# Kernel optimization log

Measured on AMD Instinct MI355X. Metric: run time of the kernel, lower is better.

The kernel has to match this reference:

```python
import jax, jax.numpy as jnp
import numpy as np

N_NODES = 50000
N_EDGES = 800000
N_FEAT = 128
HIDDEN = 64
N_GRAPHS = 256


def setup_inputs() -> dict:
    key = jax.random.key(0)
    ks = jax.random.split(key, 10)
    x = jax.random.normal(ks[0], (N_NODES, N_FEAT), dtype=jnp.float32)
    edge_index = jax.random.randint(ks[1], (2, N_EDGES), 0, N_NODES, dtype=jnp.int64)
    batch = jnp.sort(jax.random.randint(ks[2], (N_NODES,), 0, N_GRAPHS, dtype=jnp.int64))
    s1 = 1.0 / np.sqrt(N_FEAT)
    s2 = 1.0 / np.sqrt(HIDDEN)
    W1 = jax.random.normal(ks[3], (N_FEAT, HIDDEN), dtype=jnp.float32) * s1
    b1 = jnp.zeros((HIDDEN,), dtype=jnp.float32)
    W2 = jax.random.normal(ks[4], (HIDDEN, HIDDEN), dtype=jnp.float32) * s2
    b2 = jnp.zeros((HIDDEN,), dtype=jnp.float32)
    Wm1 = jax.random.normal(ks[5], (HIDDEN, HIDDEN), dtype=jnp.float32) * s2
    bm1 = jnp.zeros((HIDDEN,), dtype=jnp.float32)
    Wm2 = jax.random.normal(ks[6], (HIDDEN, 1), dtype=jnp.float32) * s2
    bm2 = jnp.zeros((1,), dtype=jnp.float32)
    return {"x": x, "edge_index": edge_index, "batch": batch,
            "W1": W1, "b1": b1, "W2": W2, "b2": b2,
            "Wm1": Wm1, "bm1": bm1, "Wm2": Wm2, "bm2": bm2}


def _gcn_layer(h, W, b, src, dst, norm, n_nodes):
    # GCNConv: h @ W, then symmetric-normalized scatter-add over edges (+ self-loops), + bias
    h = h @ W
    msg = h[src] * norm[:, None]              # [E+N, H] gather + scale
    agg = jax.ops.segment_sum(msg, dst, num_segments=n_nodes)
    return agg + b


def reference(x, edge_index, batch, W1, b1, W2, b2, Wm1, bm1, Wm2, bm2):
    n = x.shape[0]
    loops = jnp.arange(n, dtype=edge_index.dtype)
    src = jnp.concatenate([edge_index[0], loops])  # self-loops as in PyG GCNConv
    dst = jnp.concatenate([edge_index[1], loops])
    deg = jax.ops.segment_sum(jnp.ones_like(dst, dtype=x.dtype), dst, num_segments=n)
    dis = jnp.where(deg > 0, jax.lax.rsqrt(deg), 0.0)  # deg^-1/2
    norm = dis[src] * dis[dst]

    h = jax.nn.relu(_gcn_layer(x, W1, b1, src, dst, norm, n))
    h = jax.nn.relu(_gcn_layer(h, W2, b2, src, dst, norm, n))

    # global mean pool over graphs
    sums = jax.ops.segment_sum(h, batch, num_segments=N_GRAPHS)
    cnts = jax.ops.segment_sum(jnp.ones((n,), dtype=h.dtype), batch, num_segments=N_GRAPHS)
    pooled = sums / jnp.maximum(cnts, 1.0)[:, None]

    # MLP head (dropout inactive at eval)
    out = jax.nn.relu(pooled @ Wm1 + bm1) @ Wm2 + bm2
    return out.reshape(-1)
```

## Files before the change

kernel.cpp:

```cpp
#include <hip/hip_runtime.h>

#define NN 50000
#define NE 800000
#define NF 128
#define NH 64
#define NG 256
#define NB 196
#define NC 196
#define CH 4096
#define CELL 80
#define CAP 5120
#define NGB 782

typedef __attribute__((ext_vector_type(8))) short bf16x8;
typedef __attribute__((ext_vector_type(4))) float f32x4;

static __device__ __forceinline__ unsigned short f2bf(float f) {
    union { float f; unsigned u; } v; v.f = f;
    unsigned r = v.u + 0x7FFF + ((v.u >> 16) & 1);
    return (unsigned short)(r >> 16);
}
static __device__ __forceinline__ float lo16(unsigned u) {
    return __uint_as_float(u << 16);
}
static __device__ __forceinline__ float hi16(unsigned u) {
    return __uint_as_float(u & 0xFFFF0000u);
}
static __device__ __forceinline__ unsigned pack2(float a, float b) {
    return (unsigned)f2bf(a) | ((unsigned)f2bf(b) << 16);
}

__global__ __launch_bounds__(256) void prep_gemm(const int* __restrict__ ei,
                                                 int* __restrict__ histg,
                                                 int2* __restrict__ ebuf,
                                                 const float* __restrict__ X,
                                                 const float* __restrict__ W,
                                                 unsigned short* __restrict__ Y,
                                                 float* __restrict__ psum) {
    __shared__ __align__(16) char smem[35840];
    const int t = threadIdx.x;

    if (blockIdx.x < NC) {
        int* hist = (int*)smem;
        int* incl = hist + 256;
        int* lcur = incl + 256;
        int2* lpairs = (int2*)(smem + 3072);
        const int c = blockIdx.x;
        const int c0 = c * CH;

        hist[t] = 0;
        __syncthreads();

        int2 loc[16];
#pragma unroll
        for (int j = 0; j < 16; ++j) {
            int e = c0 + j * 256 + t;
            int s = -1, d = -1;
            if (e < NE) {
                s = ei[e]; d = ei[NE + e];
                atomicAdd(&hist[d >> 8], 1);
            }
            loc[j] = make_int2(s, d);
        }
        __syncthreads();

        int v = hist[t];
        incl[t] = v;
        __syncthreads();
        for (int off = 1; off < 256; off <<= 1) {
            int u = (t >= off) ? incl[t - off] : 0;
            __syncthreads();
            incl[t] += u;
            __syncthreads();
        }
        lcur[t] = incl[t] - v;
        if (t < NB) histg[c * NB + t] = v;
        __syncthreads();

#pragma unroll
        for (int j = 0; j < 16; ++j) {
            int d = loc[j].y;
            if (d >= 0) {
                int p = atomicAdd(&lcur[d >> 8], 1);
                lpairs[p] = loc[j];
            }
        }
        __syncthreads();

        const int total = incl[255];
        for (int p = t; p < total; p += 256) {
            int2 pr = lpairs[p];
            int b = pr.y >> 8;
            int i = p - (incl[b] - hist[b]);
            ebuf[(b * NC + c) * CELL + i] = pr;
        }
    } else {
        const int gb = blockIdx.x - NC;
        if (gb < 16)
            *(float4*)&psum[gb * 1024 + t * 4] = make_float4(0.f, 0.f, 0.f, 0.f);

        unsigned short* Xs = (unsigned short*)smem;
        unsigned int* Wt = (unsigned int*)(smem + 17408);
        const int base = gb * 64;

        for (int i = t * 4; i < 64 * 128; i += 1024) {
            int node = i >> 7, k = i & 127;
            int gn = base + node; if (gn >= NN) gn = NN - 1;
            float4 v = *(const float4*)&X[(size_t)gn * 128 + k];
            ushort4 o = { f2bf(v.x), f2bf(v.y), f2bf(v.z), f2bf(v.w) };
            *(ushort4*)&Xs[node * 136 + k] = o;
        }
        for (int idx = t; idx < 64 * 64; idx += 256) {
            int n = idx & 63, kp = idx >> 6;
            float w0 = W[(2 * kp) * 64 + n];
            float w1 = W[(2 * kp + 1) * 64 + n];
            Wt[n * 68 + kp] = (unsigned)f2bf(w0) | ((unsigned)f2bf(w1) << 16);
        }
        __syncthreads();

        const int w = t >> 6;
        const int lane = t & 63;
        const int l15 = lane & 15;
        const int quad = lane >> 4;
        f32x4 acc[4] = {{0.f,0.f,0.f,0.f},{0.f,0.f,0.f,0.f},{0.f,0.f,0.f,0.f},{0.f,0.f,0.f,0.f}};
#pragma unroll
        for (int kk = 0; kk < 4; ++kk) {
            const bf16x8 a = *(const bf16x8*)&Xs[(w * 16 + l15) * 136 + quad * 8 + kk * 32];
#pragma unroll
            for (int nt = 0; nt < 4; ++nt) {
                const bf16x8 b = *(const bf16x8*)&Wt[(nt * 16 + l15) * 68 + quad * 4 + kk * 16];
                acc[nt] = __builtin_amdgcn_mfma_f32_16x16x32_bf16(a, b, acc[nt], 0, 0, 0);
            }
        }
        const int r0 = base + w * 16 + quad * 4;
#pragma unroll
        for (int reg = 0; reg < 4; ++reg) {
            const int row = r0 + reg;
            if (row < NN) {
#pragma unroll
                for (int nt = 0; nt < 4; ++nt)
                    Y[(size_t)row * 64 + nt * 16 + l15] = f2bf(acc[nt][reg]);
            }
        }
    }
}

__global__ __launch_bounds__(256) void build_csr(const int2* __restrict__ ebuf,
                                                 const int* __restrict__ histg,
                                                 int2* __restrict__ row_range,
                                                 float* __restrict__ dis,
                                                 int* __restrict__ csr_src,
                                                 unsigned short* __restrict__ h) {
    const int b = blockIdx.x, t = threadIdx.x;
    const int e0 = b * CAP;
    const int node = b * 256 + t;
    __shared__ int coff[256];
    __shared__ int deg_l[256];
    __shared__ int pre[256];
    __shared__ int cur[256];
    __shared__ float sdis[256];
    __shared__ int2 lpairs[CAP];
    __shared__ int lsrc[CAP];

    int cv = (t < NB) ? histg[t * NB + b] : 0;
    coff[t] = cv;
    __syncthreads();
    for (int off = 1; off < 256; off <<= 1) {
        int u = (t >= off) ? coff[t - off] : 0;
        __syncthreads();
        coff[t] += u;
        __syncthreads();
    }
    if (cv > 0) {
        const int2* src = &ebuf[(b * NC + t) * CELL];
        int dst = coff[t] - cv;
        for (int i = 0; i < cv; ++i)
            lpairs[dst + i] = src[i];
    }
    deg_l[t] = (node < NN) ? 1 : 0;
    __syncthreads();

    const int total = coff[255];
    for (int i = t; i < total; i += 256)
        atomicAdd(&deg_l[lpairs[i].y & 255], 1);
    __syncthreads();

    int v = deg_l[t];
    pre[t] = v;
    __syncthreads();
    for (int off = 1; off < 256; off <<= 1) {
        int u = (t >= off) ? pre[t - off] : 0;
        __syncthreads();
        pre[t] += u;
        __syncthreads();
    }
    int excl = pre[t] - v;
    cur[t] = 1;
    float dv = 0.f;
    if (node < NN) {
        lsrc[excl] = node;
        row_range[node] = make_int2(e0 + excl, e0 + pre[t]);
        dv = rsqrtf((float)v);
        dis[node] = dv;
    }
    sdis[t] = dv;
    __syncthreads();
    for (int i = t; i < total; i += 256) {
        int2 p = lpairs[i];
        int d = p.y & 255;
        int pos = (pre[d] - deg_l[d]) + atomicAdd(&cur[d], 1);
        lsrc[pos] = p.x;
    }
    __syncthreads();
    const int tot_all = pre[255];
    for (int i = t; i < tot_all; i += 256)
        csr_src[e0 + i] = lsrc[i];

    const int rl0 = t >> 3;
    const int d8 = (t & 7) * 8;
#pragma unroll
    for (int c = 0; c < 8; ++c) {
        const int rl = c * 32 + rl0;
        const int n2 = b * 256 + rl;
        if (n2 < NN) {
            const float dd = sdis[rl];
            uint4 u = *(uint4*)&h[(size_t)n2 * 64 + d8];
            uint4 o;
            o.x = pack2(lo16(u.x) * dd, hi16(u.x) * dd);
            o.y = pack2(lo16(u.y) * dd, hi16(u.y) * dd);
            o.z = pack2(lo16(u.z) * dd, hi16(u.z) * dd);
            o.w = pack2(lo16(u.w) * dd, hi16(u.w) * dd);
            *(uint4*)&h[(size_t)n2 * 64 + d8] = o;
        }
    }
}

static __device__ __forceinline__ void acc8(float* acc, const uint4 u) {
    acc[0] += lo16(u.x); acc[1] += hi16(u.x);
    acc[2] += lo16(u.y); acc[3] += hi16(u.y);
    acc[4] += lo16(u.z); acc[5] += hi16(u.z);
    acc[6] += lo16(u.w); acc[7] += hi16(u.w);
}

static __device__ __forceinline__ void gather_rows(const unsigned short* __restrict__ h,
                                                   const int* __restrict__ csr_src,
                                                   int lo, int hi, int p8, float* acc) {
    int i = lo;
    for (; i + 4 <= hi; i += 4) {
        const int i0 = csr_src[i];
        const int i1 = csr_src[i + 1];
        const int i2 = csr_src[i + 2];
        const int i3 = csr_src[i + 3];
        const uint4 u0 = *(const uint4*)&h[(i0 << 6) + p8];
        const uint4 u1 = *(const uint4*)&h[(i1 << 6) + p8];
        const uint4 u2 = *(const uint4*)&h[(i2 << 6) + p8];
        const uint4 u3 = *(const uint4*)&h[(i3 << 6) + p8];
        acc8(acc, u0); acc8(acc, u1); acc8(acc, u2); acc8(acc, u3);
    }
    for (; i + 2 <= hi; i += 2) {
        const int i0 = csr_src[i];
        const int i1 = csr_src[i + 1];
        const uint4 u0 = *(const uint4*)&h[(i0 << 6) + p8];
        const uint4 u1 = *(const uint4*)&h[(i1 << 6) + p8];
        acc8(acc, u0); acc8(acc, u1);
    }
    if (i < hi) {
        const int i0 = csr_src[i];
        acc8(acc, *(const uint4*)&h[(i0 << 6) + p8]);
    }
}

__global__ __launch_bounds__(256) void agg_gemv(const unsigned short* __restrict__ h,
                                                const int2* __restrict__ row_range,
                                                const int* __restrict__ csr_src,
                                                const float* __restrict__ dis,
                                                const float* __restrict__ b1,
                                                const float* __restrict__ W2,
                                                unsigned short* __restrict__ g) {
    __shared__ unsigned short W2b[64 * 72];
    __shared__ unsigned short A[32 * 72];
    const int t = threadIdx.x;
    for (int idx = t; idx < 64 * 32; idx += 256) {
        int n = idx & 63, kp = idx >> 6;
        unsigned short w0 = f2bf(W2[(2 * kp) * 64 + n]);
        unsigned short w1 = f2bf(W2[(2 * kp + 1) * 64 + n]);
        *(unsigned*)&W2b[n * 72 + 2 * kp] = (unsigned)w0 | ((unsigned)w1 << 16);
    }

    const int base = blockIdx.x * 32;
    const int nloc = t >> 3;
    const int p8 = (t & 7) * 8;
    const int n = base + nloc;
    float acc[8] = {};
    if (n < NN) {
        const int2 rr = row_range[n];
        gather_rows(h, csr_src, rr.x, rr.y, p8, acc);
        const float dn = dis[n];
        const float4 bv0 = *(const float4*)&b1[p8];
        const float4 bv1 = *(const float4*)&b1[p8 + 4];
        acc[0] = fmaxf(acc[0] * dn + bv0.x, 0.f);
        acc[1] = fmaxf(acc[1] * dn + bv0.y, 0.f);
        acc[2] = fmaxf(acc[2] * dn + bv0.z, 0.f);
        acc[3] = fmaxf(acc[3] * dn + bv0.w, 0.f);
        acc[4] = fmaxf(acc[4] * dn + bv1.x, 0.f);
        acc[5] = fmaxf(acc[5] * dn + bv1.y, 0.f);
        acc[6] = fmaxf(acc[6] * dn + bv1.z, 0.f);
        acc[7] = fmaxf(acc[7] * dn + bv1.w, 0.f);
    }
    uint4 pk;
    pk.x = pack2(acc[0], acc[1]);
    pk.y = pack2(acc[2], acc[3]);
    pk.z = pack2(acc[4], acc[5]);
    pk.w = pack2(acc[6], acc[7]);
    *(uint4*)&A[nloc * 72 + p8] = pk;
    __syncthreads();

    const int w = t >> 6;
    const int lane = t & 63;
    const int l15 = lane & 15;
    const int quad = lane >> 4;
    const int mt = w & 1;
    const int nq = (w >> 1) * 2;
    const bf16x8 a0 = *(const bf16x8*)&A[(mt * 16 + l15) * 72 + quad * 8];
    const bf16x8 a1 = *(const bf16x8*)&A[(mt * 16 + l15) * 72 + 32 + quad * 8];
    const bf16x8 b00 = *(const bf16x8*)&W2b[(nq * 16 + l15) * 72 + quad * 8];
    const bf16x8 b01 = *(const bf16x8*)&W2b[(nq * 16 + l15) * 72 + 32 + quad * 8];
    const bf16x8 b10 = *(const bf16x8*)&W2b[((nq + 1) * 16 + l15) * 72 + quad * 8];
    const bf16x8 b11 = *(const bf16x8*)&W2b[((nq + 1) * 16 + l15) * 72 + 32 + quad * 8];
    f32x4 c0 = {0.f, 0.f, 0.f, 0.f}, c1 = {0.f, 0.f, 0.f, 0.f};
    c0 = __builtin_amdgcn_mfma_f32_16x16x32_bf16(a0, b00, c0, 0, 0, 0);
    c0 = __builtin_amdgcn_mfma_f32_16x16x32_bf16(a1, b01, c0, 0, 0, 0);
    c1 = __builtin_amdgcn_mfma_f32_16x16x32_bf16(a0, b10, c1, 0, 0, 0);
    c1 = __builtin_amdgcn_mfma_f32_16x16x32_bf16(a1, b11, c1, 0, 0, 0);
    const int r0 = base + mt * 16 + quad * 4;
    float4 d4 = *(const float4*)&dis[r0];
    const float dd[4] = { d4.x, d4.y, d4.z, d4.w };
#pragma unroll
    for (int reg = 0; reg < 4; ++reg) {
        const int row = r0 + reg;
        if (row < NN) {
            g[(size_t)row * 64 + nq * 16 + l15] = f2bf(c0[reg] * dd[reg]);
            g[(size_t)row * 64 + (nq + 1) * 16 + l15] = f2bf(c1[reg] * dd[reg]);
        }
    }
}

__global__ __launch_bounds__(256) void agg_pool(const unsigned short* __restrict__ h,
                                                const int2* __restrict__ row_range,
                                                const int* __restrict__ csr_src,
                                                const float* __restrict__ dis,
                                                const float* __restrict__ bias,
                                                const int* __restrict__ batch,
                                                float* __restrict__ psum) {
    __shared__ float rowsL[32 * 68];
    __shared__ int nb[32];
    const int t = threadIdx.x;
    const int nloc = t >> 3;
    const int n = blockIdx.x * 32 + nloc;
    const int p8 = (t & 7) * 8;
    if ((t & 7) == 0) nb[nloc] = (n < NN) ? batch[n] : -1;
    if (n < NN) {
        const int2 rr = row_range[n];
        float acc[8] = {};
        gather_rows(h, csr_src, rr.x, rr.y, p8, acc);
        const float dn = dis[n];
        const float4 bv0 = *(const float4*)&bias[p8];
        const float4 bv1 = *(const float4*)&bias[p8 + 4];
        float4 r0, r1;
        r0.x = fmaxf(acc[0] * dn + bv0.x, 0.f);
        r0.y = fmaxf(acc[1] * dn + bv0.y, 0.f);
        r0.z = fmaxf(acc[2] * dn + bv0.z, 0.f);
        r0.w = fmaxf(acc[3] * dn + bv0.w, 0.f);
        r1.x = fmaxf(acc[4] * dn + bv1.x, 0.f);
        r1.y = fmaxf(acc[5] * dn + bv1.y, 0.f);
        r1.z = fmaxf(acc[6] * dn + bv1.z, 0.f);
        r1.w = fmaxf(acc[7] * dn + bv1.w, 0.f);
        *(float4*)&rowsL[nloc * 68 + p8] = r0;
        *(float4*)&rowsL[nloc * 68 + p8 + 4] = r1;
    }
    __syncthreads();
    if (t < 64) {
        float s = 0.f; int curg = -2;
        for (int r = 0; r < 32; ++r) {
            const int gg = nb[r];
            if (gg != curg) {
                if (curg >= 0) atomicAdd(&psum[curg * 64 + t], s);
                s = 0.f; curg = gg;
            }
            if (gg >= 0) s += rowsL[r * 68 + t];
        }
        if (curg >= 0) atomicAdd(&psum[curg * 64 + t], s);
    }
}

__global__ __launch_bounds__(64) void head_kernel(const float* __restrict__ psum,
                                                  const int* __restrict__ batch,
                                                  const float* __restrict__ Wm1,
                                                  const float* __restrict__ bm1,
                                                  const float* __restrict__ Wm2,
                                                  const float* __restrict__ bm2,
                                                  float* __restrict__ out) {
    const int g = blockIdx.x;
    const int t = threadIdx.x;
    int lo = 0, hi = NN;
    while (lo < hi) { int m = (lo + hi) >> 1; if (batch[m] < g) lo = m + 1; else hi = m; }
    const int s = lo;
    hi = NN;
    while (lo < hi) { int m = (lo + hi) >> 1; if (batch[m] < g + 1) lo = m + 1; else hi = m; }
    const int cnt = lo - s;

    __shared__ float pl[64];
    pl[t] = psum[g * 64 + t] / (float)(cnt > 0 ? cnt : 1);
    __syncthreads();
    float z = bm1[t];
#pragma unroll 8
    for (int k = 0; k < 64; ++k)
        z += pl[k] * Wm1[k * 64 + t];
    z = fmaxf(z, 0.f);
    float y = z * Wm2[t];
    for (int off = 32; off; off >>= 1) y += __shfl_down(y, off);
    if (t == 0) out[g] = y + bm2[0];
}

extern "C" void kernel_launch(void* const* d_in, const int* in_sizes, int n_in,
                              void* d_out, int out_size, void* d_ws, size_t ws_size,
                              hipStream_t stream) {
    const float* x   = (const float*)d_in[0];
    const int*   ei  = (const int*)d_in[1];
    const int*   bat = (const int*)d_in[2];
    const float* W1  = (const float*)d_in[3];
    const float* b1  = (const float*)d_in[4];
    const float* W2  = (const float*)d_in[5];
    const float* b2  = (const float*)d_in[6];
    const float* Wm1 = (const float*)d_in[7];
    const float* bm1 = (const float*)d_in[8];
    const float* Wm2 = (const float*)d_in[9];
    const float* bm2 = (const float*)d_in[10];
    float* out = (float*)d_out;

    char* w = (char*)d_ws;
    int*            histg     = (int*)           (w + 0);
    int2*           row_range = (int2*)          (w + 153664);
    float*          dis       = (float*)         (w + 553664);
    int*            csr_src   = (int*)           (w + 753664);
    int2*           ebuf      = (int2*)          (w + 4767744);
    unsigned short* bufA      = (unsigned short*)(w + 29353984);
    unsigned short* bufB      = (unsigned short*)(w + 35753984);
    float*          psum      = (float*)         (w + 42153984);

    prep_gemm <<<NC + NGB, 256, 0, stream>>>(ei, histg, ebuf, x, W1, bufA, psum);
    build_csr <<<NB, 256, 0, stream>>>(ebuf, histg, row_range, dis, csr_src, bufA);
    agg_gemv  <<<(NN + 31) / 32, 256, 0, stream>>>(bufA, row_range, csr_src, dis, b1, W2, bufB);
    agg_pool  <<<(NN + 31) / 32, 256, 0, stream>>>(bufB, row_range, csr_src, dis, b2, bat, psum);
    head_kernel<<<NG, 64, 0, stream>>>(psum, bat, Wm1, bm1, Wm2, bm2, out);
}
```

Before: 155.7 us.

## Pack edge pairs to 32 bits, use wave-shuffle scans, fold source scaling into gather

Each edge pair is now stored in one 32-bit word with src in the low 16 bits and dst in the high 16 bits. This halves the traffic through the edge bucket buffer and shared memory, and the edge-index reads become int4 vector loads. The serial LDS prefix scans are replaced with wave-shuffle scans, build_csr runs with 512 threads, and W2 is packed to bf16 once by an extra prep block instead of by every agg_gemv block. The separate pass in build_csr that rescaled h by deg^-1/2 is removed, and the per-source dis factor is applied inside the layer-1 gather instead. This trades one full read-modify-write of h for an extra dis load per edge in the gather.

```diff
diff --git a/kernel.cpp b/kernel.cpp
--- a/kernel.cpp
+++ b/kernel.cpp
@@ -32,11 +32,13 @@
 
 __global__ __launch_bounds__(256) void prep_gemm(const int* __restrict__ ei,
                                                  int* __restrict__ histg,
-                                                 int2* __restrict__ ebuf,
+                                                 unsigned* __restrict__ ebuf,
                                                  const float* __restrict__ X,
                                                  const float* __restrict__ W,
+                                                 const float* __restrict__ W2,
                                                  unsigned short* __restrict__ Y,
-                                                 float* __restrict__ psum) {
+                                                 float* __restrict__ psum,
+                                                 unsigned* __restrict__ W2p) {
     __shared__ __align__(16) char smem[35840];
     const int t = threadIdx.x;
 
@@ -44,58 +46,85 @@
         int* hist = (int*)smem;
         int* incl = hist + 256;
         int* lcur = incl + 256;
-        int2* lpairs = (int2*)(smem + 3072);
+        int* wq   = lcur + 256;
+        unsigned* lpairs = (unsigned*)(smem + 4096);
         const int c = blockIdx.x;
         const int c0 = c * CH;
 
         hist[t] = 0;
         __syncthreads();
 
-        int2 loc[16];
-#pragma unroll
-        for (int j = 0; j < 16; ++j) {
-            int e = c0 + j * 256 + t;
-            int s = -1, d = -1;
-            if (e < NE) {
-                s = ei[e]; d = ei[NE + e];
-                atomicAdd(&hist[d >> 8], 1);
+        int es[16], ed[16];
+#pragma unroll
+        for (int j = 0; j < 4; ++j) {
+            const int e = c0 + (j * 256 + t) * 4;
+            int4 s4 = make_int4(-1, -1, -1, -1);
+            int4 d4 = make_int4(-1, -1, -1, -1);
+            if (e + 3 < NE) {
+                s4 = *(const int4*)&ei[e];
+                d4 = *(const int4*)&ei[NE + e];
+            } else {
+                if (e < NE)     { s4.x = ei[e];     d4.x = ei[NE + e]; }
+                if (e + 1 < NE) { s4.y = ei[e + 1]; d4.y = ei[NE + e + 1]; }
+                if (e + 2 < NE) { s4.z = ei[e + 2]; d4.z = ei[NE + e + 2]; }
             }
-            loc[j] = make_int2(s, d);
+            es[4*j] = s4.x; es[4*j+1] = s4.y; es[4*j+2] = s4.z; es[4*j+3] = s4.w;
+            ed[4*j] = d4.x; ed[4*j+1] = d4.y; ed[4*j+2] = d4.z; ed[4*j+3] = d4.w;
+            if (d4.x >= 0) atomicAdd(&hist[d4.x >> 8], 1);
+            if (d4.y >= 0) atomicAdd(&hist[d4.y >> 8], 1);
+            if (d4.z >= 0) atomicAdd(&hist[d4.z >> 8], 1);
+            if (d4.w >= 0) atomicAdd(&hist[d4.w >> 8], 1);
         }
         __syncthreads();
 
-        int v = hist[t];
-        incl[t] = v;
+        const int v = hist[t];
+        int sv = v;
+#pragma unroll
+        for (int off = 1; off < 64; off <<= 1) {
+            int u = __shfl_up(sv, off, 64);
+            if ((t & 63) >= off) sv += u;
+        }
+        if ((t & 63) == 63) wq[t >> 6] = sv;
         __syncthreads();
-        for (int off = 1; off < 256; off <<= 1) {
-            int u = (t >= off) ? incl[t - off] : 0;
-            __syncthreads();
-            incl[t] += u;
-            __syncthreads();
-        }
-        lcur[t] = incl[t] - v;
+        {
+            const int wid = t >> 6;
+            int add = 0;
+            if (wid > 0) add += wq[0];
+            if (wid > 1) add += wq[1];
+            if (wid > 2) add += wq[2];
+            sv += add;
+        }
+        incl[t] = sv;
+        lcur[t] = sv - v;
         if (t < NB) histg[c * NB + t] = v;
         __syncthreads();
 
 #pragma unroll
         for (int j = 0; j < 16; ++j) {
-            int d = loc[j].y;
+            const int d = ed[j];
             if (d >= 0) {
                 int p = atomicAdd(&lcur[d >> 8], 1);
-                lpairs[p] = loc[j];
+                lpairs[p] = (unsigned)es[j] | ((unsigned)d << 16);
             }
         }
         __syncthreads();
 
         const int total = incl[255];
         for (int p = t; p < total; p += 256) {
-            int2 pr = lpairs[p];
-            int b = pr.y >> 8;
-            int i = p - (incl[b] - hist[b]);
+            const unsigned pr = lpairs[p];
+            const int b = pr >> 24;
+            const int i = p - (incl[b] - hist[b]);
             ebuf[(b * NC + c) * CELL + i] = pr;
         }
     } else {
         const int gb = blockIdx.x - NC;
+        if (gb >= NGB) {
+            for (int idx = t; idx < 2048; idx += 256) {
+                const int n = idx >> 5, kp = idx & 31;
+                W2p[idx] = pack2(W2[(2 * kp) * 64 + n], W2[(2 * kp + 1) * 64 + n]);
+            }
+            return;
+        }
         if (gb < 16)
             *(float4*)&psum[gb * 1024 + t * 4] = make_float4(0.f, 0.f, 0.f, 0.f);
 
@@ -145,94 +174,103 @@
     }
 }
 
-__global__ __launch_bounds__(256) void build_csr(const int2* __restrict__ ebuf,
+__global__ __launch_bounds__(512) void build_csr(const unsigned* __restrict__ ebuf,
                                                  const int* __restrict__ histg,
                                                  int2* __restrict__ row_range,
                                                  float* __restrict__ dis,
-                                                 int* __restrict__ csr_src,
-                                                 unsigned short* __restrict__ h) {
+                                                 int* __restrict__ csr_src) {
     const int b = blockIdx.x, t = threadIdx.x;
     const int e0 = b * CAP;
-    const int node = b * 256 + t;
-    __shared__ int coff[256];
+    __shared__ int coffs[256];
     __shared__ int deg_l[256];
     __shared__ int pre[256];
     __shared__ int cur[256];
-    __shared__ float sdis[256];
-    __shared__ int2 lpairs[CAP];
+    __shared__ int wq[8];
+    __shared__ unsigned lpairs[CAP];
     __shared__ int lsrc[CAP];
 
-    int cv = (t < NB) ? histg[t * NB + b] : 0;
-    coff[t] = cv;
-    __syncthreads();
-    for (int off = 1; off < 256; off <<= 1) {
-        int u = (t >= off) ? coff[t - off] : 0;
-        __syncthreads();
-        coff[t] += u;
-        __syncthreads();
-    }
-    if (cv > 0) {
-        const int2* src = &ebuf[(b * NC + t) * CELL];
-        int dst = coff[t] - cv;
-        for (int i = 0; i < cv; ++i)
-            lpairs[dst + i] = src[i];
-    }
-    deg_l[t] = (node < NN) ? 1 : 0;
-    __syncthreads();
-
-    const int total = coff[255];
-    for (int i = t; i < total; i += 256)
-        atomicAdd(&deg_l[lpairs[i].y & 255], 1);
-    __syncthreads();
-
-    int v = deg_l[t];
-    pre[t] = v;
-    __syncthreads();
-    for (int off = 1; off < 256; off <<= 1) {
-        int u = (t >= off) ? pre[t - off] : 0;
-        __syncthreads();
-        pre[t] += u;
-        __syncthreads();
-    }
-    int excl = pre[t] - v;
-    cur[t] = 1;
-    float dv = 0.f;
-    if (node < NN) {
-        lsrc[excl] = node;
-        row_range[node] = make_int2(e0 + excl, e0 + pre[t]);
-        dv = rsqrtf((float)v);
-        dis[node] = dv;
-    }
-    sdis[t] = dv;
-    __syncthreads();
-    for (int i = t; i < total; i += 256) {
-        int2 p = lpairs[i];
-        int d = p.y & 255;
-        int pos = (pre[d] - deg_l[d]) + atomicAdd(&cur[d], 1);
-        lsrc[pos] = p.x;
+    int cv = 0;
+    if (t < NC) cv = histg[t * NB + b];
+    int sv = cv;
+    if (t < 256) {
+#pragma unroll
+        for (int off = 1; off < 64; off <<= 1) {
+            int u = __shfl_up(sv, off, 64);
+            if ((t & 63) >= off) sv += u;
+        }
+        if ((t & 63) == 63) wq[t >> 6] = sv;
+        deg_l[t] = (b * 256 + t < NN) ? 1 : 0;
+    }
+    __syncthreads();
+    if (t < 256) {
+        const int wid = t >> 6;
+        int add = 0;
+        if (wid > 0) add += wq[0];
+        if (wid > 1) add += wq[1];
+        if (wid > 2) add += wq[2];
+        coffs[t] = sv + add;
+    }
+    __syncthreads();
+
+    if (t < NC && cv > 0) {
+        const uint4* src4 = (const uint4*)&ebuf[(size_t)(b * NC + t) * CELL];
+        const int dst = coffs[t] - cv;
+        for (int i = 0; i < cv; i += 4) {
+            const uint4 u = src4[i >> 2];
+            lpairs[dst + i] = u.x;
+            if (i + 1 < cv) lpairs[dst + i + 1] = u.y;
+            if (i + 2 < cv) lpairs[dst + i + 2] = u.z;
+            if (i + 3 < cv) lpairs[dst + i + 3] = u.w;
+        }
+    }
+    __syncthreads();
+
+    const int total = coffs[255];
+    for (int i = t; i < total; i += 512)
+        atomicAdd(&deg_l[(lpairs[i] >> 16) & 255], 1);
+    __syncthreads();
+
+    int dvi = 0, psv = 0;
+    if (t < 256) {
+        dvi = deg_l[t];
+        psv = dvi;
+#pragma unroll
+        for (int off = 1; off < 64; off <<= 1) {
+            int u = __shfl_up(psv, off, 64);
+            if ((t & 63) >= off) psv += u;
+        }
+        if ((t & 63) == 63) wq[4 + (t >> 6)] = psv;
+    }
+    __syncthreads();
+    if (t < 256) {
+        const int wid = t >> 6;
+        int add = 0;
+        if (wid > 0) add += wq[4];
+        if (wid > 1) add += wq[5];
+        if (wid > 2) add += wq[6];
+        psv += add;
+        pre[t] = psv;
+        cur[t] = 1;
+        const int nd = b * 256 + t;
+        if (nd < NN) {
+            const int excl = psv - dvi;
+            lsrc[excl] = nd;
+            row_range[nd] = make_int2(e0 + excl, e0 + psv);
+            dis[nd] = rsqrtf((float)dvi);
+        }
+    }
+    __syncthreads();
+
+    for (int i = t; i < total; i += 512) {
+        const unsigned p = lpairs[i];
+        const int d = (p >> 16) & 255;
+        const int pos = (pre[d] - deg_l[d]) + atomicAdd(&cur[d], 1);
+        lsrc[pos] = (int)(p & 0xFFFFu);
     }
     __syncthreads();
     const int tot_all = pre[255];
-    for (int i = t; i < tot_all; i += 256)
+    for (int i = t; i < tot_all; i += 512)
         csr_src[e0 + i] = lsrc[i];
-
-    const int rl0 = t >> 3;
-    const int d8 = (t & 7) * 8;
-#pragma unroll
-    for (int c = 0; c < 8; ++c) {
-        const int rl = c * 32 + rl0;
-        const int n2 = b * 256 + rl;
-        if (n2 < NN) {
-            const float dd = sdis[rl];
-            uint4 u = *(uint4*)&h[(size_t)n2 * 64 + d8];
-            uint4 o;
-            o.x = pack2(lo16(u.x) * dd, hi16(u.x) * dd);
-            o.y = pack2(lo16(u.y) * dd, hi16(u.y) * dd);
-            o.z = pack2(lo16(u.z) * dd, hi16(u.z) * dd);
-            o.w = pack2(lo16(u.w) * dd, hi16(u.w) * dd);
-            *(uint4*)&h[(size_t)n2 * 64 + d8] = o;
-        }
-    }
 }
 
 static __device__ __forceinline__ void acc8(float* acc, const uint4 u) {
@@ -240,6 +278,12 @@
     acc[2] += lo16(u.y); acc[3] += hi16(u.y);
     acc[4] += lo16(u.z); acc[5] += hi16(u.z);
     acc[6] += lo16(u.w); acc[7] += hi16(u.w);
+}
+static __device__ __forceinline__ void fma8(float* acc, const uint4 u, const float d) {
+    acc[0] = fmaf(lo16(u.x), d, acc[0]); acc[1] = fmaf(hi16(u.x), d, acc[1]);
+    acc[2] = fmaf(lo16(u.y), d, acc[2]); acc[3] = fmaf(hi16(u.y), d, acc[3]);
+    acc[4] = fmaf(lo16(u.z), d, acc[4]); acc[5] = fmaf(hi16(u.z), d, acc[5]);
+    acc[6] = fmaf(lo16(u.w), d, acc[6]); acc[7] = fmaf(hi16(u.w), d, acc[7]);
 }
 
 static __device__ __forceinline__ void gather_rows(const unsigned short* __restrict__ h,
@@ -270,21 +314,51 @@
     }
 }
 
+static __device__ __forceinline__ void gather_rows_scaled(const unsigned short* __restrict__ h,
+                                                          const int* __restrict__ csr_src,
+                                                          const float* __restrict__ dis,
+                                                          int lo, int hi, int p8, float* acc) {
+    int i = lo;
+    for (; i + 4 <= hi; i += 4) {
+        const int i0 = csr_src[i];
+        const int i1 = csr_src[i + 1];
+        const int i2 = csr_src[i + 2];
+        const int i3 = csr_src[i + 3];
+        const float d0 = dis[i0], d1 = dis[i1], d2 = dis[i2], d3 = dis[i3];
+        const uint4 u0 = *(const uint4*)&h[(i0 << 6) + p8];
+        const uint4 u1 = *(const uint4*)&h[(i1 << 6) + p8];
+        const uint4 u2 = *(const uint4*)&h[(i2 << 6) + p8];
+        const uint4 u3 = *(const uint4*)&h[(i3 << 6) + p8];
+        fma8(acc, u0, d0); fma8(acc, u1, d1); fma8(acc, u2, d2); fma8(acc, u3, d3);
+    }
+    for (; i + 2 <= hi; i += 2) {
+        const int i0 = csr_src[i];
+        const int i1 = csr_src[i + 1];
+        const float d0 = dis[i0], d1 = dis[i1];
+        const uint4 u0 = *(const uint4*)&h[(i0 << 6) + p8];
+        const uint4 u1 = *(const uint4*)&h[(i1 << 6) + p8];
+        fma8(acc, u0, d0); fma8(acc, u1, d1);
+    }
+    if (i < hi) {
+        const int i0 = csr_src[i];
+        const float d0 = dis[i0];
+        fma8(acc, *(const uint4*)&h[(i0 << 6) + p8], d0);
+    }
+}
+
 __global__ __launch_bounds__(256) void agg_gemv(const unsigned short* __restrict__ h,
                                                 const int2* __restrict__ row_range,
                                                 const int* __restrict__ csr_src,
                                                 const float* __restrict__ dis,
                                                 const float* __restrict__ b1,
-                                                const float* __restrict__ W2,
+                                                const unsigned* __restrict__ W2p,
                                                 unsigned short* __restrict__ g) {
     __shared__ unsigned short W2b[64 * 72];
     __shared__ unsigned short A[32 * 72];
     const int t = threadIdx.x;
-    for (int idx = t; idx < 64 * 32; idx += 256) {
-        int n = idx & 63, kp = idx >> 6;
-        unsigned short w0 = f2bf(W2[(2 * kp) * 64 + n]);
-        unsigned short w1 = f2bf(W2[(2 * kp + 1) * 64 + n]);
-        *(unsigned*)&W2b[n * 72 + 2 * kp] = (unsigned)w0 | ((unsigned)w1 << 16);
+    for (int idx = t; idx < 2048; idx += 256) {
+        const int n = idx >> 5, kp = idx & 31;
+        *(unsigned*)&W2b[n * 72 + 2 * kp] = W2p[idx];
     }
 
     const int base = blockIdx.x * 32;
@@ -294,7 +368,7 @@
     float acc[8] = {};
     if (n < NN) {
         const int2 rr = row_range[n];
-        gather_rows(h, csr_src, rr.x, rr.y, p8, acc);
+        gather_rows_scaled(h, csr_src, dis, rr.x, rr.y, p8, acc);
         const float dn = dis[n];
         const float4 bv0 = *(const float4*)&b1[p8];
         const float4 bv1 = *(const float4*)&b1[p8 + 4];
@@ -443,14 +517,15 @@
     int2*           row_range = (int2*)          (w + 153664);
     float*          dis       = (float*)         (w + 553664);
     int*            csr_src   = (int*)           (w + 753664);
-    int2*           ebuf      = (int2*)          (w + 4767744);
-    unsigned short* bufA      = (unsigned short*)(w + 29353984);
-    unsigned short* bufB      = (unsigned short*)(w + 35753984);
-    float*          psum      = (float*)         (w + 42153984);
-
-    prep_gemm <<<NC + NGB, 256, 0, stream>>>(ei, histg, ebuf, x, W1, bufA, psum);
-    build_csr <<<NB, 256, 0, stream>>>(ebuf, histg, row_range, dis, csr_src, bufA);
-    agg_gemv  <<<(NN + 31) / 32, 256, 0, stream>>>(bufA, row_range, csr_src, dis, b1, W2, bufB);
+    unsigned*       ebuf      = (unsigned*)      (w + 4767744);
+    unsigned short* bufA      = (unsigned short*)(w + 17060864);
+    unsigned short* bufB      = (unsigned short*)(w + 23460864);
+    float*          psum      = (float*)         (w + 29860864);
+    unsigned*       W2p       = (unsigned*)      (w + 29926400);
+
+    prep_gemm <<<NC + NGB + 1, 256, 0, stream>>>(ei, histg, ebuf, x, W1, W2, bufA, psum, W2p);
+    build_csr <<<NB, 512, 0, stream>>>(ebuf, histg, row_range, dis, csr_src);
+    agg_gemv  <<<(NN + 31) / 32, 256, 0, stream>>>(bufA, row_range, csr_src, dis, b1, W2p, bufB);
     agg_pool  <<<(NN + 31) / 32, 256, 0, stream>>>(bufB, row_range, csr_src, dis, b2, bat, psum);
     head_kernel<<<NG, 64, 0, stream>>>(psum, bat, Wm1, bm1, Wm2, bm2, out);
 }
```

New measurement: 149.7 us. 3.9% less time.
